# Performance work log

Hardware: AMD Instinct MI355X
Metric: run time of the kernel (lower is better)

The kernel has to match this reference:

```python
import jax, jax.numpy as jnp
import numpy as np

IN_FILTERS = 512
SIM_DIM = 128
LOOKUP = 101
OUT_DIM = 128


def setup_inputs() -> dict:
    key = jax.random.key(0)
    k1, k2, k3, k4 = jax.random.split(key, 4)
    x = jax.random.normal(k1, (4, IN_FILTERS, 1024, 8, 8), dtype=jnp.float32)
    # nn.Linear weights: [out, in]
    W_proj = jax.random.normal(k2, (SIM_DIM, IN_FILTERS), dtype=jnp.float32) * (1.0 / np.sqrt(IN_FILTERS))
    W_fc = jax.random.normal(k3, (OUT_DIM, LOOKUP), dtype=jnp.float32) * (1.0 / np.sqrt(LOOKUP))
    b_fc = jax.random.normal(k4, (OUT_DIM,), dtype=jnp.float32) * 0.01
    return {"x": x, "W_proj": W_proj, "W_fc": W_fc, "b_fc": b_fc}


def reference(x, W_proj, W_fc, b_fc):
    # x: [B, C, T, H, W]; inputs list has a single entry here, cat is identity
    feat = jnp.mean(x, axis=(3, 4))              # [B, C, T]
    feat = jnp.transpose(feat, (0, 2, 1))        # [B, T, C]
    p = jnp.einsum('btc,dc->btd', feat, W_proj)  # projection, no bias
    # F.normalize(p, p=2, dim=2) with eps=1e-12
    norm = jnp.linalg.norm(p, axis=2, keepdims=True)
    p = p / jnp.maximum(norm, 1e-12)
    B, T, _ = p.shape
    sim = jnp.einsum('btd,bsd->bts', p, p)       # full TxT similarity [B,T,T]
    half = (LOOKUP - 1) // 2
    sim_pad = jnp.pad(sim, ((0, 0), (0, 0), (half, half)))
    # band gather: row t takes padded cols [t, t+LOOKUP)
    cols = jnp.arange(T)[:, None] + jnp.arange(LOOKUP)[None, :]  # [T, L]
    band = sim_pad[:, jnp.arange(T)[:, None], cols]              # [B, T, L]
    out = jnp.einsum('btl,ol->bto', band, W_fc) + b_fc
    return jax.nn.relu(out)
```

## Files before the change

kernel.cpp:

```cpp
#include <hip/hip_runtime.h>
#include <cstdint>
#include <cstddef>

#define B_DIM 4
#define C_DIM 512
#define T_DIM 1024
#define D_DIM 128
#define L_DIM 101
#define O_DIM 128

__global__ __launch_bounds__(256) void wpt_kernel(const float* __restrict__ Wp,
                                                  float* __restrict__ WpT) {
    const int idx = blockIdx.x * 256 + threadIdx.x;
    const int c = idx >> 7;
    const int d = idx & 127;
    WpT[idx] = Wp[d * C_DIM + c];
}

#define ROWS 4
__global__ __launch_bounds__(256) void pool_proj_kernel(const float* __restrict__ x,
                                                        const float* __restrict__ WpT,
                                                        float* __restrict__ p) {
    __shared__ float feat_s[ROWS * C_DIM];
    __shared__ float red_s[8 * ROWS * D_DIM];
    __shared__ float nrm_s[ROWS * 2];
    const int tid = threadIdx.x;
    const int bt0 = blockIdx.x * ROWS;
    const int b   = bt0 >> 10;
    const int t0  = bt0 & (T_DIM - 1);

    {
        const int g    = tid >> 2;
        const int sub4 = tid & 3;
        #pragma unroll 2
        for (int it = 0; it < (ROWS * C_DIM) / 64; ++it) {
            const int idx = it * 64 + g;
            const int row = idx >> 9;
            const int c   = idx & (C_DIM - 1);
            const float* src =
                x + ((((size_t)b * C_DIM + c) * T_DIM + (t0 + row)) << 6) + (sub4 << 2);
            const float4 v0 = *(const float4*)(src + 0);
            const float4 v1 = *(const float4*)(src + 16);
            const float4 v2 = *(const float4*)(src + 32);
            const float4 v3 = *(const float4*)(src + 48);
            float s = (v0.x + v0.y + v0.z + v0.w) + (v1.x + v1.y + v1.z + v1.w)
                    + (v2.x + v2.y + v2.z + v2.w) + (v3.x + v3.y + v3.z + v3.w);
            s += __shfl_xor(s, 1, 4);
            s += __shfl_xor(s, 2, 4);
            if (sub4 == 0) feat_s[idx] = s * (1.0f / 64.0f);
        }
    }
    __syncthreads();

    {
        const int lane4 = (tid & 31) << 2;
        const int strm  = tid >> 5;
        float a0[4] = {0,0,0,0}, a1[4] = {0,0,0,0}, a2[4] = {0,0,0,0}, a3[4] = {0,0,0,0};
        for (int ci = 0; ci < C_DIM / 8; ++ci) {
            const int c = ci * 8 + strm;
            const float4 w = *(const float4*)(WpT + (size_t)c * D_DIM + lane4);
            const float f0 = feat_s[0 * C_DIM + c];
            const float f1 = feat_s[1 * C_DIM + c];
            const float f2 = feat_s[2 * C_DIM + c];
            const float f3 = feat_s[3 * C_DIM + c];
            a0[0] += f0 * w.x; a0[1] += f0 * w.y; a0[2] += f0 * w.z; a0[3] += f0 * w.w;
            a1[0] += f1 * w.x; a1[1] += f1 * w.y; a1[2] += f1 * w.z; a1[3] += f1 * w.w;
            a2[0] += f2 * w.x; a2[1] += f2 * w.y; a2[2] += f2 * w.z; a2[3] += f2 * w.w;
            a3[0] += f3 * w.x; a3[1] += f3 * w.y; a3[2] += f3 * w.z; a3[3] += f3 * w.w;
        }
        float* rb = red_s + strm * (ROWS * D_DIM) + lane4;
        *(float4*)(rb + 0 * D_DIM) = make_float4(a0[0], a0[1], a0[2], a0[3]);
        *(float4*)(rb + 1 * D_DIM) = make_float4(a1[0], a1[1], a1[2], a1[3]);
        *(float4*)(rb + 2 * D_DIM) = make_float4(a2[0], a2[1], a2[2], a2[3]);
        *(float4*)(rb + 3 * D_DIM) = make_float4(a3[0], a3[1], a3[2], a3[3]);
    }
    __syncthreads();

    float pv[2];
    const int lane = tid & 63;
    const int wv   = tid >> 6;
    #pragma unroll
    for (int j = 0; j < 2; ++j) {
        const int idx = j * 256 + tid;
        float v = 0.f;
        #pragma unroll
        for (int s = 0; s < 8; ++s) v += red_s[s * (ROWS * D_DIM) + idx];
        pv[j] = v;
        float ss = v * v;
        ss += __shfl_xor(ss, 32, 64);
        ss += __shfl_xor(ss, 16, 64);
        ss += __shfl_xor(ss,  8, 64);
        ss += __shfl_xor(ss,  4, 64);
        ss += __shfl_xor(ss,  2, 64);
        ss += __shfl_xor(ss,  1, 64);
        if (lane == 0) {
            const int row  = (j * 4 + wv) >> 1;
            const int half = wv & 1;
            nrm_s[row * 2 + half] = ss;
        }
    }
    __syncthreads();
    #pragma unroll
    for (int j = 0; j < 2; ++j) {
        const int idx = j * 256 + tid;
        const int row = idx >> 7;
        const int d   = idx & 127;
        const float ss  = nrm_s[row * 2] + nrm_s[row * 2 + 1];
        const float inv = 1.0f / fmaxf(sqrtf(ss), 1e-12f);
        p[(size_t)(bt0 + row) * D_DIM + d] = pv[j] * inv;
    }
}

#define TT 8
#define PS 132
#define NR 109
#define FS 108
#define SMEM_F (TT * FS + O_DIM * FS)

__global__ __launch_bounds__(256) void band_fc_kernel(const float* __restrict__ p,
                                                      const float* __restrict__ Wfc,
                                                      const float* __restrict__ bfc,
                                                      float* __restrict__ out) {
    __shared__ float smem[SMEM_F];
    float* p_s = smem;
    const int tid = threadIdx.x;
    const int b   = blockIdx.x >> 7;
    const int t0  = (blockIdx.x & 127) * TT;

    for (int idx = tid; idx < NR * (D_DIM / 4); idx += 256) {
        const int i  = idx >> 5;
        const int k4 = (idx & 31) << 2;
        const int r  = t0 - 50 + i;
        float4 v = make_float4(0.f, 0.f, 0.f, 0.f);
        if (r >= 0 && r < T_DIM)
            v = *(const float4*)(p + (size_t)((b << 10) + r) * D_DIM + k4);
        *(float4*)(p_s + i * PS + k4) = v;
    }
    __syncthreads();

    float c00 = 0.f, c01 = 0.f, c10 = 0.f, c11 = 0.f;
    const bool active = tid < 4 * 51;
    const int tp = active ? (tid / 51) : 0;
    const int lq = active ? (tid - tp * 51) : 0;
    {
        const float* pa0  = p_s + (2 * tp + 50) * PS;
        const float* pa1  = pa0 + PS;
        const float* pb00 = p_s + (2 * tp + lq) * PS;
        const float* pb01 = pb00 + PS;
        const float* pb10 = p_s + (2 * tp + lq + 51) * PS;
        const float* pb11 = pb10 + PS;
        #pragma unroll 4
        for (int k = 0; k < D_DIM; k += 4) {
            const float4 a0 = *(const float4*)(pa0 + k);
            const float4 a1 = *(const float4*)(pa1 + k);
            const float4 b0 = *(const float4*)(pb00 + k);
            const float4 b1 = *(const float4*)(pb01 + k);
            const float4 b2 = *(const float4*)(pb10 + k);
            const float4 b3 = *(const float4*)(pb11 + k);
            c00 += a0.x * b0.x + a0.y * b0.y + a0.z * b0.z + a0.w * b0.w;
            c01 += a1.x * b1.x + a1.y * b1.y + a1.z * b1.z + a1.w * b1.w;
            c10 += a0.x * b2.x + a0.y * b2.y + a0.z * b2.z + a0.w * b2.w;
            c11 += a1.x * b3.x + a1.y * b3.y + a1.z * b3.z + a1.w * b3.w;
        }
    }
    __syncthreads();

    float* band_s = smem;
    float* wfc_s  = smem + TT * FS;
    if (active) {
        band_s[(2 * tp + 0) * FS + lq] = c00;
        band_s[(2 * tp + 1) * FS + lq] = c01;
        if (lq < 50) {
            band_s[(2 * tp + 0) * FS + lq + 51] = c10;
            band_s[(2 * tp + 1) * FS + lq + 51] = c11;
        }
    }
    for (int i = tid; i < TT * 7; i += 256) {
        const int t = i / 7;
        band_s[t * FS + L_DIM + (i - t * 7)] = 0.f;
    }
    for (int i = tid; i < O_DIM * L_DIM; i += 256) {
        const int o = i / L_DIM;
        wfc_s[o * FS + (i - o * L_DIM)] = Wfc[i];
    }
    for (int i = tid; i < O_DIM * 7; i += 256) {
        const int o = i / 7;
        wfc_s[o * FS + L_DIM + (i - o * 7)] = 0.f;
    }
    __syncthreads();

    const int o  = tid & 127;
    const int th = tid >> 7;
    const float bias = bfc[o];
    float acc0 = bias, acc1 = bias, acc2 = bias, acc3 = bias;
    const float* w  = wfc_s + o * FS;
    const float* bd = band_s + (th * 4) * FS;
    #pragma unroll 4
    for (int k = 0; k < 104; k += 4) {
        const float4 wv = *(const float4*)(w + k);
        const float4 b0 = *(const float4*)(bd + 0 * FS + k);
        const float4 b1 = *(const float4*)(bd + 1 * FS + k);
        const float4 b2 = *(const float4*)(bd + 2 * FS + k);
        const float4 b3 = *(const float4*)(bd + 3 * FS + k);
        acc0 += wv.x * b0.x + wv.y * b0.y + wv.z * b0.z + wv.w * b0.w;
        acc1 += wv.x * b1.x + wv.y * b1.y + wv.z * b1.z + wv.w * b1.w;
        acc2 += wv.x * b2.x + wv.y * b2.y + wv.z * b2.z + wv.w * b2.w;
        acc3 += wv.x * b3.x + wv.y * b3.y + wv.z * b3.z + wv.w * b3.w;
    }
    const size_t obase = (size_t)((b << 10) + t0 + th * 4) * O_DIM + o;
    out[obase + 0 * O_DIM] = fmaxf(acc0, 0.f);
    out[obase + 1 * O_DIM] = fmaxf(acc1, 0.f);
    out[obase + 2 * O_DIM] = fmaxf(acc2, 0.f);
    out[obase + 3 * O_DIM] = fmaxf(acc3, 0.f);
}

extern "C" void kernel_launch(void* const* d_in, const int* in_sizes, int n_in,
                              void* d_out, int out_size, void* d_ws, size_t ws_size,
                              hipStream_t stream) {
    const float* x   = (const float*)d_in[0];
    const float* Wp  = (const float*)d_in[1];
    const float* Wfc = (const float*)d_in[2];
    const float* bfc = (const float*)d_in[3];
    float* out = (float*)d_out;

    char* ws = (char*)d_ws;
    float* WpT = (float*)(ws);
    float* p   = (float*)(ws + (size_t)1024 * 1024);

    wpt_kernel<<<(C_DIM * D_DIM) / 256, 256, 0, stream>>>(Wp, WpT);
    pool_proj_kernel<<<(B_DIM * T_DIM) / ROWS, 256, 0, stream>>>(x, WpT, p);
    band_fc_kernel<<<B_DIM * (T_DIM / TT), 256, 0, stream>>>(p, Wfc, bfc, out);
}
```

Measured before the change: 702.8 us.

## Split pooling into a separate contiguous-read kernel feeding the projection

Average pooling now runs in its own kernel. Each block reads long contiguous spans of x per channel and transposes through shared memory into a [B,T,C] feature buffer. The projection kernel then loads its features from that buffer with vector loads. The aim is better DRAM streaming on the dominant read of x, at the cost of an extra intermediate write and read plus one more launch.

```diff
diff --git a/kernel.cpp b/kernel.cpp
--- a/kernel.cpp
+++ b/kernel.cpp
@@ -17,38 +17,62 @@
     WpT[idx] = Wp[d * C_DIM + c];
 }
 
+#define PC 16
+#define PT 128
+__global__ __launch_bounds__(256) void pool_kernel(const float* __restrict__ x,
+                                                   float* __restrict__ feat) {
+    __shared__ float fs[PC][PT + 1];
+    const int tid = threadIdx.x;
+    const int bid = blockIdx.x;
+    const int b   = bid >> 8;
+    const int cc  = (bid >> 3) & 31;
+    const int tt  = bid & 7;
+    const int c0  = cc * PC;
+    const int t0  = tt * PT;
+
+    #pragma unroll 4
+    for (int it = 0; it < 32; ++it) {
+        const int g  = it * 256 + tid;
+        const int cl = g >> 9;
+        const int wi = g & 511;
+        const float* src = x + ((size_t)(b * C_DIM + c0 + cl) * T_DIM + t0) * 64
+                             + (size_t)wi * 16;
+        const float4 v0 = *(const float4*)(src + 0);
+        const float4 v1 = *(const float4*)(src + 4);
+        const float4 v2 = *(const float4*)(src + 8);
+        const float4 v3 = *(const float4*)(src + 12);
+        float s = (v0.x + v0.y + v0.z + v0.w) + (v1.x + v1.y + v1.z + v1.w)
+                + (v2.x + v2.y + v2.z + v2.w) + (v3.x + v3.y + v3.z + v3.w);
+        s += __shfl_xor(s, 1, 4);
+        s += __shfl_xor(s, 2, 4);
+        if ((tid & 3) == 0) fs[cl][wi >> 2] = s * (1.0f / 64.0f);
+    }
+    __syncthreads();
+
+    #pragma unroll
+    for (int j = 0; j < (PC * PT) / 256; ++j) {
+        const int idx = j * 256 + tid;
+        const int t   = idx >> 4;
+        const int cl  = idx & 15;
+        feat[((size_t)(b << 10) + t0 + t) * C_DIM + c0 + cl] = fs[cl][t];
+    }
+}
+
 #define ROWS 4
-__global__ __launch_bounds__(256) void pool_proj_kernel(const float* __restrict__ x,
-                                                        const float* __restrict__ WpT,
-                                                        float* __restrict__ p) {
-    __shared__ float feat_s[ROWS * C_DIM];
+__global__ __launch_bounds__(256) void proj_kernel(const float* __restrict__ feat,
+                                                   const float* __restrict__ WpT,
+                                                   float* __restrict__ p) {
+    __shared__ __align__(16) float feat_s[ROWS * C_DIM];
     __shared__ float red_s[8 * ROWS * D_DIM];
     __shared__ float nrm_s[ROWS * 2];
     const int tid = threadIdx.x;
     const int bt0 = blockIdx.x * ROWS;
-    const int b   = bt0 >> 10;
-    const int t0  = bt0 & (T_DIM - 1);
 
     {
-        const int g    = tid >> 2;
-        const int sub4 = tid & 3;
-        #pragma unroll 2
-        for (int it = 0; it < (ROWS * C_DIM) / 64; ++it) {
-            const int idx = it * 64 + g;
-            const int row = idx >> 9;
-            const int c   = idx & (C_DIM - 1);
-            const float* src =
-                x + ((((size_t)b * C_DIM + c) * T_DIM + (t0 + row)) << 6) + (sub4 << 2);
-            const float4 v0 = *(const float4*)(src + 0);
-            const float4 v1 = *(const float4*)(src + 16);
-            const float4 v2 = *(const float4*)(src + 32);
-            const float4 v3 = *(const float4*)(src + 48);
-            float s = (v0.x + v0.y + v0.z + v0.w) + (v1.x + v1.y + v1.z + v1.w)
-                    + (v2.x + v2.y + v2.z + v2.w) + (v3.x + v3.y + v3.z + v3.w);
-            s += __shfl_xor(s, 1, 4);
-            s += __shfl_xor(s, 2, 4);
-            if (sub4 == 0) feat_s[idx] = s * (1.0f / 64.0f);
-        }
+        const float4* src = (const float4*)(feat + (size_t)bt0 * C_DIM);
+        float4* dst = (float4*)feat_s;
+        dst[tid]       = src[tid];
+        dst[256 + tid] = src[256 + tid];
     }
     __syncthreads();
 
@@ -224,10 +248,12 @@
     float* out = (float*)d_out;
 
     char* ws = (char*)d_ws;
-    float* WpT = (float*)(ws);
-    float* p   = (float*)(ws + (size_t)1024 * 1024);
-
-    wpt_kernel<<<(C_DIM * D_DIM) / 256, 256, 0, stream>>>(Wp, WpT);
-    pool_proj_kernel<<<(B_DIM * T_DIM) / ROWS, 256, 0, stream>>>(x, WpT, p);
+    float* WpT  = (float*)(ws);
+    float* p    = (float*)(ws + (size_t)1024 * 1024);
+    float* feat = (float*)(ws + (size_t)4 * 1024 * 1024);
+
+    wpt_kernel <<<(C_DIM * D_DIM) / 256, 256, 0, stream>>>(Wp, WpT);
+    pool_kernel<<<B_DIM * 32 * 8, 256, 0, stream>>>(x, feat);
+    proj_kernel<<<(B_DIM * T_DIM) / ROWS, 256, 0, stream>>>(feat, WpT, p);
     band_fc_kernel<<<B_DIM * (T_DIM / TT), 256, 0, stream>>>(p, Wfc, bfc, out);
 }
```

New measurement: 718.9 us. +2.3%, slower.
